# Kernel tuning notes

Measured on AMD Instinct MI355X. Metric: run time of the kernel, lower is better.

The kernel has to match this reference:

```python
import jax, jax.numpy as jnp
import numpy as np

NUM_HEADS = 32
NUM_KV_HEADS = 2
HEAD_DIM = 128
ROTARY_DIM = 64  # partial_rotary_factor 0.5 * head_dim
HIDDEN = 4096
SEQ = 2048


def _rotate_half_interleaved(x):
    # rotates pairs (x0,x1)->(-x1,x0) interleaved, matching torch rotate_half above
    x1 = x[..., 0::2]
    x2 = x[..., 1::2]
    return jnp.stack((-x2, x1), axis=-1).reshape(x.shape)


def _apply_rope(q, k, cos, sin):
    # q: [S, Hq, D], k: [S, Hkv, D], cos/sin: [S, ROTARY_DIM]
    # torch code: take first half of cos/sin then repeat_interleave(2) -> length ROTARY_DIM
    cos_i = jnp.repeat(cos[:, : ROTARY_DIM // 2], 2, axis=-1)[:, None, :]  # [S,1,RD]
    sin_i = jnp.repeat(sin[:, : ROTARY_DIM // 2], 2, axis=-1)[:, None, :]
    q_rot, q_pass = q[..., :ROTARY_DIM], q[..., ROTARY_DIM:]
    k_rot, k_pass = k[..., :ROTARY_DIM], k[..., ROTARY_DIM:]
    q_rot = q_rot * cos_i + _rotate_half_interleaved(q_rot) * sin_i
    k_rot = k_rot * cos_i + _rotate_half_interleaved(k_rot) * sin_i
    return jnp.concatenate([q_rot, q_pass], -1), jnp.concatenate([k_rot, k_pass], -1)


def setup_inputs() -> dict:
    key = jax.random.key(0)
    ks = jax.random.split(key, 6)
    S = SEQ
    qkv_out = (NUM_HEADS + 2 * NUM_KV_HEADS) * HEAD_DIM  # 4608
    hidden_states = jax.random.normal(ks[0], (S, HIDDEN), jnp.float32)
    # realistic rope angles
    inv_freq = 1.0 / (10000.0 ** (np.arange(0, ROTARY_DIM, 2, dtype=np.float32) / ROTARY_DIM))
    ang = np.arange(S, dtype=np.float32)[:, None] * inv_freq[None, :]  # [S, RD/2]
    ang = np.concatenate([ang, ang], axis=-1)  # [S, RD]
    cos = jnp.asarray(np.cos(ang))
    sin = jnp.asarray(np.sin(ang))
    w_qkv = jax.random.normal(ks[1], (HIDDEN, qkv_out), jnp.float32) * 0.02
    b_qkv = jax.random.normal(ks[2], (qkv_out,), jnp.float32) * 0.02
    w_o = jax.random.normal(ks[3], (NUM_HEADS * HEAD_DIM, HIDDEN), jnp.float32) * 0.02
    return {"hidden_states": hidden_states, "cos": cos, "sin": sin,
            "w_qkv": w_qkv, "b_qkv": b_qkv, "w_o": w_o}


def reference(hidden_states, cos, sin, w_qkv, b_qkv, w_o):
    S = hidden_states.shape[0]
    qkv = hidden_states @ w_qkv + b_qkv  # [S, 4608]
    nq = NUM_HEADS * HEAD_DIM
    nkv = NUM_KV_HEADS * HEAD_DIM
    q = qkv[:, :nq].reshape(S, NUM_HEADS, HEAD_DIM)
    k = qkv[:, nq:nq + nkv].reshape(S, NUM_KV_HEADS, HEAD_DIM)
    v = qkv[:, nq + nkv:].reshape(S, NUM_KV_HEADS, HEAD_DIM)
    q, k = _apply_rope(q, k, cos, sin)
    # GQA: repeat kv heads to match q heads
    rep = NUM_HEADS // NUM_KV_HEADS
    k = jnp.repeat(k, rep, axis=1)  # [S, Hq, D]
    v = jnp.repeat(v, rep, axis=1)
    scale = 1.0 / jnp.sqrt(jnp.asarray(HEAD_DIM, q.dtype))
    scores = jnp.einsum("qhd,khd->hqk", q, k) * scale  # [H, S, S]
    causal = jnp.tril(jnp.ones((S, S), bool))
    scores = jnp.where(causal[None], scores, jnp.asarray(-1e30, scores.dtype))
    probs = jax.nn.softmax(scores, axis=-1)
    attn = jnp.einsum("hqk,khd->qhd", probs, v).reshape(S, NUM_HEADS * HEAD_DIM)
    return attn @ w_o  # [S, HIDDEN]
```

## Files before the change

kernel.cpp:

```cpp
#include <hip/hip_runtime.h>
#include <stdint.h>

#define SEQ    2048
#define HIDDEN 4096
#define NQH    32
#define NKVH   2
#define HD     128
#define QKVN   4608
#define ATTN_N 4096

typedef short bf16x8 __attribute__((ext_vector_type(8)));
typedef float f32x4  __attribute__((ext_vector_type(4)));

#define ASYNC16(gp, lp) __builtin_amdgcn_global_load_lds( \
    (const __attribute__((address_space(1))) void*)(gp),  \
    (__attribute__((address_space(3))) void*)(lp), 16, 0, 0)

#define MFMA16(a, b, c) __builtin_amdgcn_mfma_f32_16x16x32_bf16((a), (b), (c), 0, 0, 0)

__device__ __forceinline__ float bf2f(unsigned short u) {
  union { unsigned int i; float f; } v; v.i = ((unsigned int)u) << 16; return v.f;
}
__device__ __forceinline__ unsigned short f2bf(float f) {
  union { float f; unsigned int i; } v; v.f = f;
  unsigned int r = v.i + 0x7fffu + ((v.i >> 16) & 1u);
  return (unsigned short)(r >> 16);
}

__global__ void detect_dtype(const unsigned short* __restrict__ hs, int* __restrict__ flag) {
  int bad = 0;
  for (int i = 0; i < 128; i += 2) {
    const int e = (hs[i] >> 7) & 0xFF;
    if (e < 100 || e > 140) bad++;
  }
  *flag = (bad > 16) ? 1 : 0;
}

__global__ void to_bf16_any(const void* __restrict__ in, unsigned short* __restrict__ out,
                            int n4, const int* __restrict__ flag) {
  const int i = blockIdx.x * blockDim.x + threadIdx.x;
  if (i >= n4) return;
  if (*flag) {
    const float4 f = ((const float4*)in)[i];
    ushort4 u; u.x = f2bf(f.x); u.y = f2bf(f.y); u.z = f2bf(f.z); u.w = f2bf(f.w);
    ((ushort4*)out)[i] = u;
  } else {
    ((ushort4*)out)[i] = ((const ushort4*)in)[i];
  }
}

__global__ void to_f32_any(const void* __restrict__ in, float* __restrict__ out,
                           int n4, const int* __restrict__ flag) {
  const int i = blockIdx.x * blockDim.x + threadIdx.x;
  if (i >= n4) return;
  if (*flag) {
    ((float4*)out)[i] = ((const float4*)in)[i];
  } else {
    const ushort4 u = ((const ushort4*)in)[i];
    float4 f; f.x = bf2f(u.x); f.y = bf2f(u.y); f.z = bf2f(u.z); f.w = bf2f(u.w);
    ((float4*)out)[i] = f;
  }
}

__global__ void transpose_any(const void* __restrict__ in, unsigned short* __restrict__ out,
                              int R, int C, const int* __restrict__ flag) {
  __shared__ unsigned short t[32][36];
  const int r0 = blockIdx.y * 32, c0 = blockIdx.x * 32;
  const int lr = threadIdx.x >> 3;
  const int lc = (threadIdx.x & 7) << 2;
  unsigned short v0, v1, v2, v3;
  if (*flag) {
    const float4 f = *(const float4*)((const float*)in + (size_t)(r0 + lr) * C + c0 + lc);
    v0 = f2bf(f.x); v1 = f2bf(f.y); v2 = f2bf(f.z); v3 = f2bf(f.w);
  } else {
    const ushort4 u = *(const ushort4*)((const unsigned short*)in + (size_t)(r0 + lr) * C + c0 + lc);
    v0 = u.x; v1 = u.y; v2 = u.z; v3 = u.w;
  }
  t[lr][lc] = v0; t[lr][lc + 1] = v1; t[lr][lc + 2] = v2; t[lr][lc + 3] = v3;
  __syncthreads();
  unsigned short* op = out + (size_t)(c0 + lr) * R + r0 + lc;
  ushort4 w;
  w.x = t[lc][lr]; w.y = t[lc + 1][lr]; w.z = t[lc + 2][lr]; w.w = t[lc + 3][lr];
  *(ushort4*)op = w;
}

__global__ __launch_bounds__(512, 2)
void gemm_bt_2ph(const unsigned short* __restrict__ A,
                 const unsigned short* __restrict__ Bt,
                 const float* __restrict__ bias,
                 void* __restrict__ C,
                 int M, int N, int K, const int* __restrict__ of32) {
  __shared__ __attribute__((aligned(16))) unsigned short lds[49152];
  const int tid  = threadIdx.x;
  const int wave = tid >> 6, lane = tid & 63;
  const int quad = lane >> 4, l16 = lane & 15;

  const int nwg = gridDim.x * gridDim.y;
  int bid = blockIdx.y * gridDim.x + blockIdx.x;
  bid = (bid & 7) * (nwg >> 3) + (bid >> 3);
  const int bx = bid % gridDim.x, by = bid / gridDim.x;
  const int m0 = by * 256, n0 = bx * 128;

  const int wm = (wave >> 1) * 64, wn = (wave & 1) * 64;

  const int srow = tid >> 2;
  const int g8   = (((tid & 3) ^ ((srow >> 1) & 3)) << 3);
  const unsigned short* gA = A  + (size_t)(m0 + srow) * K + g8;
  const unsigned short* gB = Bt + (size_t)(n0 + srow) * K + g8;
  const size_t rstep = (size_t)128 * K;

  const int rsw   = ((quad ^ ((l16 >> 1) & 3)) << 3);
  const int aBase = (wm + l16) * 32 + rsw;
  const int bBase = 8192 + (wn + l16) * 32 + rsw;

  f32x4 acc[4][4] = {};
  const int nt = K >> 6;

#define STAGEA(bufb, kh, kb) do {                                              \
    const unsigned short* _s = gA + (kb) + ((kh) << 5);                        \
    unsigned short* _d = &lds[(bufb) * 24576 + (kh) * 12288 + tid * 8];        \
    ASYNC16(_s, _d);                                                           \
    ASYNC16(_s + rstep, _d + 4096);                                            \
  } while (0)
#define STAGEB(bufb, kh, kb) do {                                              \
    const unsigned short* _s = gB + (kb) + ((kh) << 5);                        \
    unsigned short* _d = &lds[(bufb) * 24576 + (kh) * 12288 + 8192 + tid * 8]; \
    ASYNC16(_s, _d);                                                           \
  } while (0)
#define BARX() do { asm volatile("" ::: "memory");          \
    __builtin_amdgcn_s_barrier();                           \
    asm volatile("" ::: "memory"); } while (0)

  STAGEA(0, 0, 0); STAGEB(0, 0, 0);
  STAGEA(0, 1, 0); STAGEB(0, 1, 0);
  asm volatile("s_waitcnt vmcnt(3)" ::: "memory");
  BARX();

  for (int t = 0; t < nt; ++t) {
    const int b = t & 1, nb = b ^ 1;
    const int kb1 = (t + 1) << 6;
    const bool pf = (t + 1 < nt);

    {
      const int cb = b * 24576;
      bf16x8 af[4], bfr[4];
#pragma unroll
      for (int i = 0; i < 4; i++) af[i]  = *(const bf16x8*)&lds[cb + aBase + i * 512];
#pragma unroll
      for (int j = 0; j < 4; j++) bfr[j] = *(const bf16x8*)&lds[cb + bBase + j * 512];
      if (pf) { STAGEA(nb, 0, kb1); STAGEB(nb, 0, kb1); }
      BARX();
      __builtin_amdgcn_s_setprio(1);
#pragma unroll
      for (int i = 0; i < 4; i++)
#pragma unroll
        for (int j = 0; j < 4; j++) acc[i][j] = MFMA16(af[i], bfr[j], acc[i][j]);
      __builtin_amdgcn_s_setprio(0);
      if (pf) asm volatile("s_waitcnt vmcnt(3)" ::: "memory");
      else    asm volatile("s_waitcnt vmcnt(0)" ::: "memory");
      BARX();
    }

    {
      const int cb = b * 24576 + 12288;
      bf16x8 af[4], bfr[4];
#pragma unroll
      for (int i = 0; i < 4; i++) af[i]  = *(const bf16x8*)&lds[cb + aBase + i * 512];
#pragma unroll
      for (int j = 0; j < 4; j++) bfr[j] = *(const bf16x8*)&lds[cb + bBase + j * 512];
      if (pf) { STAGEA(nb, 1, kb1); STAGEB(nb, 1, kb1); }
      BARX();
      __builtin_amdgcn_s_setprio(1);
#pragma unroll
      for (int i = 0; i < 4; i++)
#pragma unroll
        for (int j = 0; j < 4; j++) acc[i][j] = MFMA16(af[i], bfr[j], acc[i][j]);
      __builtin_amdgcn_s_setprio(0);
      if (pf) {
        asm volatile("s_waitcnt vmcnt(3)" ::: "memory");
        BARX();
      }
    }
  }
#undef STAGEA
#undef STAGEB
#undef BARX

  const int wf32 = of32 ? *of32 : 0;
#pragma unroll
  for (int j = 0; j < 4; j++) {
    const int col = n0 + wn + j * 16 + l16;
    const float bv = bias ? bias[col] : 0.0f;
#pragma unroll
    for (int i = 0; i < 4; i++) {
#pragma unroll
      for (int r = 0; r < 4; r++) {
        const int row = m0 + wm + i * 16 + quad * 4 + r;
        const float v = acc[i][j][r] + bv;
        const size_t off = (size_t)row * N + col;
        if (wf32) ((float*)C)[off] = v;
        else      ((unsigned short*)C)[off] = f2bf(v);
      }
    }
  }
}

__global__ void rope_split(const unsigned short* __restrict__ qkv,
                           const float* __restrict__ cosb,
                           const float* __restrict__ sinb,
                           unsigned short* __restrict__ qb,
                           unsigned short* __restrict__ kb,
                           unsigned short* __restrict__ vtb) {
  const int s = blockIdx.x;
  const unsigned short* row = qkv + (size_t)s * QKVN;
  const float sc = 0.08838834764831845f * 1.44269504088896341f;
  for (int p = threadIdx.x; p < QKVN / 2; p += blockDim.x) {
    const int col = p << 1;
    const int head = col >> 7;
    const int d = col & 127;
    float x0 = bf2f(row[col]), x1 = bf2f(row[col + 1]);
    float y0 = x0, y1 = x1;
    if (d < 64) {
      const float c  = cosb[s * 64 + (d >> 1)];
      const float sn = sinb[s * 64 + (d >> 1)];
      y0 = x0 * c - x1 * sn;
      y1 = x1 * c + x0 * sn;
    }
    if (head < NQH) {
      const size_t o = (size_t)head * SEQ * HD + (size_t)s * HD + d;
      qb[o] = f2bf(y0 * sc); qb[o + 1] = f2bf(y1 * sc);
    } else if (head < NQH + NKVH) {
      const size_t o = (size_t)(head - NQH) * SEQ * HD + (size_t)s * HD + d;
      kb[o] = f2bf(y0); kb[o + 1] = f2bf(y1);
    } else {
      const size_t o = (size_t)(head - NQH - NKVH) * HD * SEQ + (size_t)d * SEQ + s;
      vtb[o] = f2bf(x0); vtb[o + SEQ] = f2bf(x1);
    }
  }
}

__global__ __launch_bounds__(256, 3)
void attn_fwd(const unsigned short* __restrict__ qb,
              const unsigned short* __restrict__ kb,
              const unsigned short* __restrict__ vtb,
              unsigned short* __restrict__ ob) {
  const int h = blockIdx.x;
  const int qt = 31 - (int)blockIdx.y;
  const int tid = threadIdx.x;
  const int wave = tid >> 6, lane = tid & 63;
  const int quad = lane >> 4, l16 = lane & 15;
  const int q0 = qt * 64 + wave * 16;
  const unsigned short* qh  = qb  + (size_t)h * SEQ * HD;
  const unsigned short* kh  = kb  + (size_t)(h >> 4) * SEQ * HD;
  const unsigned short* vth = vtb + (size_t)(h >> 4) * HD * SEQ;

  __shared__ __attribute__((aligned(16))) unsigned short Ks[64 * 128];
  __shared__ __attribute__((aligned(16))) unsigned short Vs[128 * 64];
  __shared__ __attribute__((aligned(16))) unsigned short plds[4][16][80];

  bf16x8 qf[4];
#pragma unroll
  for (int kbk = 0; kbk < 4; kbk++)
    qf[kbk] = *(const bf16x8*)&qh[(size_t)(q0 + l16) * HD + kbk * 32 + quad * 8];

  bf16x8 onesf;
#pragma unroll
  for (int i = 0; i < 8; i++) onesf[i] = (short)0x3F80;

  f32x4 oacc[8] = {};
  f32x4 lacc = {};
  float mrow[4] = {-1e30f, -1e30f, -1e30f, -1e30f};

  for (int kt = 0; kt <= qt; kt++) {
    const int kbase = kt * 64;
    __syncthreads();
#pragma unroll
    for (int c = 0; c < 4; c++) {
      const int j = c * 256 + tid;
      const int key = j >> 4;
      const int g = (j & 15) ^ (key & 15);
      ASYNC16(kh + (size_t)(kbase + key) * HD + g * 8, (unsigned short*)Ks + j * 8);
    }
#pragma unroll
    for (int c = 0; c < 4; c++) {
      const int j = c * 256 + tid;
      const int d = j >> 3;
      const int g = (j & 7) ^ (d & 7);
      ASYNC16(vth + (size_t)d * SEQ + kbase + g * 8, (unsigned short*)Vs + j * 8);
    }
    __syncthreads();

    f32x4 sv[4] = {};
#pragma unroll
    for (int kbk = 0; kbk < 4; kbk++) {
#pragma unroll
      for (int t = 0; t < 4; t++) {
        bf16x8 kf = *(const bf16x8*)&Ks[(t * 16 + l16) * 128 + (((kbk << 2) + quad) ^ l16) * 8];
        sv[t] = __builtin_amdgcn_mfma_f32_16x16x32_bf16(qf[kbk], kf, sv[t], 0, 0, 0);
      }
    }
    if (kt == qt) {
#pragma unroll
      for (int t = 0; t < 4; t++) {
        const int key = kbase + t * 16 + l16;
#pragma unroll
        for (int r = 0; r < 4; r++)
          if (key > q0 + quad * 4 + r) sv[t][r] = -1e30f;
      }
    }
    float alpha[4];
#pragma unroll
    for (int r = 0; r < 4; r++) {
      float mx = fmaxf(fmaxf(sv[0][r], sv[1][r]), fmaxf(sv[2][r], sv[3][r]));
#pragma unroll
      for (int off = 8; off; off >>= 1) mx = fmaxf(mx, __shfl_xor(mx, off));
      const float mnew = fmaxf(mrow[r], mx);
      alpha[r] = __builtin_exp2f(mrow[r] - mnew);
      mrow[r] = mnew;
#pragma unroll
      for (int t = 0; t < 4; t++)
        sv[t][r] = __builtin_exp2f(sv[t][r] - mnew);
    }
#pragma unroll
    for (int dt = 0; dt < 8; dt++)
#pragma unroll
      for (int r = 0; r < 4; r++) oacc[dt][r] *= alpha[r];
#pragma unroll
    for (int r = 0; r < 4; r++) lacc[r] *= alpha[r];
    __syncthreads();
#pragma unroll
    for (int r = 0; r < 4; r++)
#pragma unroll
      for (int t = 0; t < 4; t++)
        plds[wave][quad * 4 + r][t * 16 + l16] = f2bf(sv[t][r]);
    __syncthreads();
    bf16x8 pf0 = *(const bf16x8*)&plds[wave][l16][quad * 8];
    bf16x8 pf1 = *(const bf16x8*)&plds[wave][l16][32 + quad * 8];
    lacc = __builtin_amdgcn_mfma_f32_16x16x32_bf16(pf0, onesf, lacc, 0, 0, 0);
    lacc = __builtin_amdgcn_mfma_f32_16x16x32_bf16(pf1, onesf, lacc, 0, 0, 0);
#pragma unroll
    for (int dt = 0; dt < 8; dt++) {
      const int vrow = (dt * 16 + l16) * 64;
      bf16x8 vf0 = *(const bf16x8*)&Vs[vrow + ((quad) ^ (l16 & 7)) * 8];
      oacc[dt] = __builtin_amdgcn_mfma_f32_16x16x32_bf16(pf0, vf0, oacc[dt], 0, 0, 0);
      bf16x8 vf1 = *(const bf16x8*)&Vs[vrow + ((4 + quad) ^ (l16 & 7)) * 8];
      oacc[dt] = __builtin_amdgcn_mfma_f32_16x16x32_bf16(pf1, vf1, oacc[dt], 0, 0, 0);
    }
  }
#pragma unroll
  for (int dt = 0; dt < 8; dt++) {
#pragma unroll
    for (int r = 0; r < 4; r++) {
      const float v = oacc[dt][r] / lacc[r];
      ob[(size_t)(q0 + quad * 4 + r) * ATTN_N + h * HD + dt * 16 + l16] = f2bf(v);
    }
  }
}

extern "C" void kernel_launch(void* const* d_in, const int* in_sizes, int n_in,
                              void* d_out, int out_size, void* d_ws, size_t ws_size,
                              hipStream_t stream) {
  const void* hs_raw   = d_in[0];
  const void* cos_raw  = d_in[1];
  const void* sin_raw  = d_in[2];
  const void* wqkv_raw = d_in[3];
  const void* bqkv_raw = d_in[4];
  const void* wo_raw   = d_in[5];
  unsigned short* ws = (unsigned short*)d_ws;

  unsigned short* R1   = ws;
  unsigned short* R2   = R1 + (size_t)QKVN * HIDDEN;
  unsigned short* hs_c = R2 + (size_t)SEQ * QKVN;
  float* cosf  = (float*)(hs_c + (size_t)SEQ * HIDDEN);
  float* sinf  = cosf + SEQ * 64;
  float* biasf = sinf + SEQ * 64;
  int*   flag  = (int*)(biasf + QKVN);

  unsigned short* wt_qkv = R1;
  unsigned short* qbuf   = R1;
  unsigned short* kbuf   = qbuf + (size_t)NQH * SEQ * HD;
  unsigned short* vtbuf  = kbuf + (size_t)NKVH * SEQ * HD;
  unsigned short* wt_o   = R1;
  unsigned short* qkv    = R2;
  unsigned short* attnb  = R2;

  detect_dtype<<<1, 1, 0, stream>>>((const unsigned short*)hs_raw, flag);
  to_bf16_any<<<(SEQ * HIDDEN / 4 + 255) / 256, 256, 0, stream>>>(hs_raw, hs_c, SEQ * HIDDEN / 4, flag);
  to_f32_any<<<(SEQ * 64 / 4 + 255) / 256, 256, 0, stream>>>(cos_raw, cosf, SEQ * 64 / 4, flag);
  to_f32_any<<<(SEQ * 64 / 4 + 255) / 256, 256, 0, stream>>>(sin_raw, sinf, SEQ * 64 / 4, flag);
  to_f32_any<<<(QKVN / 4 + 255) / 256, 256, 0, stream>>>(bqkv_raw, biasf, QKVN / 4, flag);

  transpose_any<<<dim3(QKVN / 32, HIDDEN / 32), 256, 0, stream>>>(wqkv_raw, wt_qkv, HIDDEN, QKVN, flag);
  gemm_bt_2ph<<<dim3(QKVN / 128, SEQ / 256), 512, 0, stream>>>(hs_c, wt_qkv, biasf, qkv, SEQ, QKVN, HIDDEN, nullptr);
  rope_split<<<SEQ, 256, 0, stream>>>(qkv, cosf, sinf, qbuf, kbuf, vtbuf);
  attn_fwd<<<dim3(NQH, SEQ / 64), 256, 0, stream>>>(qbuf, kbuf, vtbuf, attnb);
  transpose_any<<<dim3(ATTN_N / 32, HIDDEN / 32), 256, 0, stream>>>(wo_raw, wt_o, HIDDEN, ATTN_N, flag);
  gemm_bt_2ph<<<dim3(ATTN_N / 128, SEQ / 256), 512, 0, stream>>>(attnb, wt_o, nullptr, d_out, SEQ, ATTN_N, HIDDEN, flag);
}
```

Measured before the change: 531.4 us.

## Restructure GEMM into triple-buffered K=32 pipeline with prefetch distance two

Replaces the double-buffered GEMM, which split each 64-wide K tile into two halves, with a three-slot ring of 32-wide K tiles that prefetches two steps ahead. LDS per block drops from 96KB to 72KB and launch bounds are raised to 4 blocks per SM, with the aim of more latency hiding and higher occupancy. The cost is twice as many loop iterations, each with two barriers, and more register pressure under the tighter launch bound.

```diff
diff --git a/kernel.cpp b/kernel.cpp
--- a/kernel.cpp
+++ b/kernel.cpp
@@ -84,13 +84,13 @@
   *(ushort4*)op = w;
 }
 
-__global__ __launch_bounds__(512, 2)
-void gemm_bt_2ph(const unsigned short* __restrict__ A,
-                 const unsigned short* __restrict__ Bt,
-                 const float* __restrict__ bias,
-                 void* __restrict__ C,
-                 int M, int N, int K, const int* __restrict__ of32) {
-  __shared__ __attribute__((aligned(16))) unsigned short lds[49152];
+__global__ __launch_bounds__(512, 4)
+void gemm_bt_p3(const unsigned short* __restrict__ A,
+                const unsigned short* __restrict__ Bt,
+                const float* __restrict__ bias,
+                void* __restrict__ C,
+                int M, int N, int K, const int* __restrict__ of32) {
+  __shared__ __attribute__((aligned(16))) unsigned short lds[36864];
   const int tid  = threadIdx.x;
   const int wave = tid >> 6, lane = tid & 63;
   const int quad = lane >> 4, l16 = lane & 15;
@@ -109,81 +109,50 @@
   const unsigned short* gB = Bt + (size_t)(n0 + srow) * K + g8;
   const size_t rstep = (size_t)128 * K;
 
-  const int rsw   = ((quad ^ ((l16 >> 1) & 3)) << 3);
-  const int aBase = (wm + l16) * 32 + rsw;
-  const int bBase = 8192 + (wn + l16) * 32 + rsw;
+  const int rsw  = ((quad ^ ((l16 >> 1) & 3)) << 3);
+  const int aOff = (wm + l16) * 32 + rsw;
+  const int bOff = 8192 + (wn + l16) * 32 + rsw;
 
   f32x4 acc[4][4] = {};
-  const int nt = K >> 6;
-
-#define STAGEA(bufb, kh, kb) do {                                              \
-    const unsigned short* _s = gA + (kb) + ((kh) << 5);                        \
-    unsigned short* _d = &lds[(bufb) * 24576 + (kh) * 12288 + tid * 8];        \
-    ASYNC16(_s, _d);                                                           \
-    ASYNC16(_s + rstep, _d + 4096);                                            \
-  } while (0)
-#define STAGEB(bufb, kh, kb) do {                                              \
-    const unsigned short* _s = gB + (kb) + ((kh) << 5);                        \
-    unsigned short* _d = &lds[(bufb) * 24576 + (kh) * 12288 + 8192 + tid * 8]; \
-    ASYNC16(_s, _d);                                                           \
+  const int nt = K >> 5;
+
+#define STAGE(bo, kb) do {                                   \
+    unsigned short* _d = &lds[(bo) + tid * 8];               \
+    ASYNC16(gA + (kb), _d);                                  \
+    ASYNC16(gA + rstep + (kb), _d + 4096);                   \
+    ASYNC16(gB + (kb), _d + 8192);                           \
   } while (0)
 #define BARX() do { asm volatile("" ::: "memory");          \
     __builtin_amdgcn_s_barrier();                           \
     asm volatile("" ::: "memory"); } while (0)
 
-  STAGEA(0, 0, 0); STAGEB(0, 0, 0);
-  STAGEA(0, 1, 0); STAGEB(0, 1, 0);
+  STAGE(0,     0);
+  STAGE(12288, 32);
   asm volatile("s_waitcnt vmcnt(3)" ::: "memory");
   BARX();
 
+  int bo0 = 0, bo1 = 12288, bo2 = 24576;
   for (int t = 0; t < nt; ++t) {
-    const int b = t & 1, nb = b ^ 1;
-    const int kb1 = (t + 1) << 6;
-    const bool pf = (t + 1 < nt);
-
-    {
-      const int cb = b * 24576;
-      bf16x8 af[4], bfr[4];
-#pragma unroll
-      for (int i = 0; i < 4; i++) af[i]  = *(const bf16x8*)&lds[cb + aBase + i * 512];
-#pragma unroll
-      for (int j = 0; j < 4; j++) bfr[j] = *(const bf16x8*)&lds[cb + bBase + j * 512];
-      if (pf) { STAGEA(nb, 0, kb1); STAGEB(nb, 0, kb1); }
-      BARX();
-      __builtin_amdgcn_s_setprio(1);
-#pragma unroll
-      for (int i = 0; i < 4; i++)
-#pragma unroll
-        for (int j = 0; j < 4; j++) acc[i][j] = MFMA16(af[i], bfr[j], acc[i][j]);
-      __builtin_amdgcn_s_setprio(0);
-      if (pf) asm volatile("s_waitcnt vmcnt(3)" ::: "memory");
-      else    asm volatile("s_waitcnt vmcnt(0)" ::: "memory");
-      BARX();
-    }
-
-    {
-      const int cb = b * 24576 + 12288;
-      bf16x8 af[4], bfr[4];
-#pragma unroll
-      for (int i = 0; i < 4; i++) af[i]  = *(const bf16x8*)&lds[cb + aBase + i * 512];
-#pragma unroll
-      for (int j = 0; j < 4; j++) bfr[j] = *(const bf16x8*)&lds[cb + bBase + j * 512];
-      if (pf) { STAGEA(nb, 1, kb1); STAGEB(nb, 1, kb1); }
-      BARX();
-      __builtin_amdgcn_s_setprio(1);
-#pragma unroll
-      for (int i = 0; i < 4; i++)
-#pragma unroll
-        for (int j = 0; j < 4; j++) acc[i][j] = MFMA16(af[i], bfr[j], acc[i][j]);
-      __builtin_amdgcn_s_setprio(0);
-      if (pf) {
-        asm volatile("s_waitcnt vmcnt(3)" ::: "memory");
-        BARX();
-      }
-    }
-  }
-#undef STAGEA
-#undef STAGEB
+    bf16x8 af[4], bfr[4];
+#pragma unroll
+    for (int i = 0; i < 4; i++) af[i]  = *(const bf16x8*)&lds[bo0 + aOff + i * 512];
+#pragma unroll
+    for (int j = 0; j < 4; j++) bfr[j] = *(const bf16x8*)&lds[bo0 + bOff + j * 512];
+    const bool pf = (t + 2 < nt);
+    if (pf) STAGE(bo2, (t + 2) << 5);
+    BARX();
+    __builtin_amdgcn_s_setprio(1);
+#pragma unroll
+    for (int i = 0; i < 4; i++)
+#pragma unroll
+      for (int j = 0; j < 4; j++) acc[i][j] = MFMA16(af[i], bfr[j], acc[i][j]);
+    __builtin_amdgcn_s_setprio(0);
+    if (pf) asm volatile("s_waitcnt vmcnt(3)" ::: "memory");
+    else    asm volatile("s_waitcnt vmcnt(0)" ::: "memory");
+    BARX();
+    const int tmp = bo0; bo0 = bo1; bo1 = bo2; bo2 = tmp;
+  }
+#undef STAGE
 #undef BARX
 
   const int wf32 = of32 ? *of32 : 0;
@@ -391,9 +360,9 @@
   to_f32_any<<<(QKVN / 4 + 255) / 256, 256, 0, stream>>>(bqkv_raw, biasf, QKVN / 4, flag);
 
   transpose_any<<<dim3(QKVN / 32, HIDDEN / 32), 256, 0, stream>>>(wqkv_raw, wt_qkv, HIDDEN, QKVN, flag);
-  gemm_bt_2ph<<<dim3(QKVN / 128, SEQ / 256), 512, 0, stream>>>(hs_c, wt_qkv, biasf, qkv, SEQ, QKVN, HIDDEN, nullptr);
+  gemm_bt_p3<<<dim3(QKVN / 128, SEQ / 256), 512, 0, stream>>>(hs_c, wt_qkv, biasf, qkv, SEQ, QKVN, HIDDEN, nullptr);
   rope_split<<<SEQ, 256, 0, stream>>>(qkv, cosf, sinf, qbuf, kbuf, vtbuf);
   attn_fwd<<<dim3(NQH, SEQ / 64), 256, 0, stream>>>(qbuf, kbuf, vtbuf, attnb);
   transpose_any<<<dim3(ATTN_N / 32, HIDDEN / 32), 256, 0, stream>>>(wo_raw, wt_o, HIDDEN, ATTN_N, flag);
-  gemm_bt_2ph<<<dim3(ATTN_N / 128, SEQ / 256), 512, 0, stream>>>(attnb, wt_o, nullptr, d_out, SEQ, ATTN_N, HIDDEN, flag);
-}
+  gemm_bt_p3<<<dim3(ATTN_N / 128, SEQ / 256), 512, 0, stream>>>(attnb, wt_o, nullptr, d_out, SEQ, ATTN_N, HIDDEN, flag);
+}
```

Measured after the change: 500.4 us. 1.06x faster.
